# Kernel tuning notes

Measured on AMD Instinct MI355X. Metric: run time of the kernel, lower is better.

The kernel has to match this reference:

```python
import jax, jax.numpy as jnp
import numpy as np
from jax import lax

H_STEP = 1.0 / 3.0  # h = (t1 - t0) / N with t0=0, t1=1, N=3
N_STEPS = 3


def _conv(x, w):
    # x: [B, C, H, W], w: [O, I, kh, kw], 'same' padding, stride 1
    return lax.conv_general_dilated(
        x, w, window_strides=(1, 1), padding='SAME',
        dimension_numbers=('NCHW', 'OIHW', 'NCHW'))


def setup_inputs() -> dict:
    key = jax.random.key(0)
    ks = jax.random.split(key, 5)
    B, C, H, W = 16, 128, 128, 128
    fan_in = C * 9
    return {
        'x': jax.random.normal(ks[0], (B, C, H, W), dtype=jnp.float32),
        'w1': jax.random.normal(ks[1], (C, C, 3, 3), dtype=jnp.float32) * (2.0 / fan_in) ** 0.5,
        'b1': jax.random.normal(ks[2], (C,), dtype=jnp.float32) * 0.01,
        'w2': jax.random.normal(ks[3], (C, C, 3, 3), dtype=jnp.float32) * (2.0 / fan_in) ** 0.5,
        'b2': jax.random.normal(ks[4], (C,), dtype=jnp.float32) * 0.01,
    }


def reference(x, w1, b1, w2, b2):
    # Euler-step residual block: x <- x + h * conv2(relu(conv1(x))) for N steps
    for _ in range(N_STEPS):
        t = jax.nn.relu(_conv(x, w1) + b1[None, :, None, None])
        x = x + H_STEP * (_conv(t, w2) + b2[None, :, None, None])
    return jax.nn.relu(x)
```

## Files before the change

kernel.cpp:

```cpp
#include <hip/hip_runtime.h>
#include <hip/hip_bf16.h>


#define BATCH 16
#define CH    128
#define HH    128
#define WW    128
#define H_STEP (1.0f/3.0f)

typedef short bf16x8 __attribute__((ext_vector_type(8)));
typedef float f32x4  __attribute__((ext_vector_type(4)));

__device__ __forceinline__ float bf2f(unsigned short u) {
    union { unsigned int i; float f; } c; c.i = ((unsigned int)u) << 16; return c.f;
}
__device__ __forceinline__ unsigned short f2bf(float f) {
    union { float f; unsigned int i; } c; c.f = f;
    unsigned int i = c.i;
    return (unsigned short)((i + 0x7FFFu + ((i >> 16) & 1u)) >> 16);
}

__device__ __forceinline__ void gload16(const unsigned short* g, unsigned short* l) {
    __builtin_amdgcn_global_load_lds(
        (const __attribute__((address_space(1))) unsigned int*)g,
        (__attribute__((address_space(3))) unsigned int*)l, 16, 0, 0);
}

__global__ __launch_bounds__(256)
void transpose_x(const float* __restrict__ x, unsigned short* __restrict__ xb)
{
    __shared__ unsigned short s[128 * 132];
    const int tid = threadIdx.x;
    const int bz  = blockIdx.x;
    const int b = bz >> 7, y = bz & 127;

    #pragma unroll
    for (int it = 0; it < 16; ++it) {
        int idx = it * 256 + tid;
        int ci = idx >> 5, xq = idx & 31;
        float4 v = *(const float4*)&x[(((size_t)b * CH + ci) * HH + y) * WW + xq * 4];
        uint2 p;
        p.x = (unsigned int)f2bf(v.x) | ((unsigned int)f2bf(v.y) << 16);
        p.y = (unsigned int)f2bf(v.z) | ((unsigned int)f2bf(v.w) << 16);
        *(uint2*)&s[ci * 132 + xq * 4] = p;
    }
    __syncthreads();
    #pragma unroll
    for (int it = 0; it < 8; ++it) {
        int idx = it * 256 + tid;
        int xx = idx >> 4, cc = idx & 15;
        unsigned short t[8];
        #pragma unroll
        for (int k = 0; k < 8; ++k) t[k] = s[(cc * 8 + k) * 132 + xx];
        uint4 p;
        p.x = (unsigned int)t[0] | ((unsigned int)t[1] << 16);
        p.y = (unsigned int)t[2] | ((unsigned int)t[3] << 16);
        p.z = (unsigned int)t[4] | ((unsigned int)t[5] << 16);
        p.w = (unsigned int)t[6] | ((unsigned int)t[7] << 16);
        *(uint4*)&xb[((size_t)(b * HH + y) * WW + xx) * CH + cc * 8] = p;
    }
}

__global__ __launch_bounds__(256)
void convert_w(const float* __restrict__ w, unsigned short* __restrict__ wb)
{
    int idx = blockIdx.x * 256 + threadIdx.x;
    #pragma unroll
    for (int t = 0; t < 9; ++t)
        wb[t * 16384 + idx] = f2bf(w[(size_t)idx * 9 + t]);
}

template<int MODE>
__global__ __launch_bounds__(256, 2)
void conv_mfma(const unsigned short* __restrict__ in,
               const unsigned short* __restrict__ wb,
               const float* __restrict__ bias,
               const unsigned short* resb,
               unsigned short* outb,
               float* __restrict__ outf)
{
    __shared__ unsigned short s_in[130 * CH];
    __shared__ unsigned short s_w [2][128 * 64];

    const int tid = threadIdx.x;
    const int bz0 = blockIdx.x;
    const int bz  = ((bz0 & 7) << 8) | (bz0 >> 3);
    const int b = bz >> 7, y = bz & 127;

    const int lane = tid & 63;
    const int wid  = tid >> 6;
    const int woc0 = (wid >> 1) * 64;
    const int wpx0 = (wid & 1) * 64;
    const int n16  = lane & 15;
    const int q    = lane >> 4;

    const int wr   = lane >> 3;
    const int wc   = lane & 7;
    const int w_lane_elem = wr * CH + ((wc ^ wr) << 3);
    const int xl   = lane >> 4;
    const int ch16 = lane & 15;

    const int kylo = (y == 0)      ? 1 : 0;
    const int kyhi = (y == HH - 1) ? 1 : 2;
    const int NS   = (kyhi - kylo + 1) * 6;

    f32x4 acc[4][4];
    #pragma unroll
    for (int i = 0; i < 4; ++i)
        #pragma unroll
        for (int j = 0; j < 4; ++j) acc[i][j] = (f32x4)0.0f;

    if (tid < 32) {
        int r  = (tid < 16) ? 0 : 129;
        int cc = tid & 15;
        uint4 z = {0u, 0u, 0u, 0u};
        *(uint4*)&s_in[r * CH + cc * 8] = z;
    }

    auto stage_in = [&](int gy) {
        const size_t inrow = ((size_t)(b * HH + gy) * WW) * CH;
        #pragma unroll
        for (int c = 0; c < 8; ++c) {
            int x   = wid * 32 + c * 4 + xl;
            int swz = (x + 1) & 7;
            const unsigned short* src = in + inrow + (size_t)x * CH + ((ch16 ^ swz) << 3);
            unsigned short* dst = (unsigned short*)s_in + CH + (wid * 8 + c) * 512;
            gload16(src, dst);
        }
    };
    auto stage_w = [&](int tap, int kh, int buf) {
        const unsigned short* wt = wb + tap * 16384 + kh * 64;
        #pragma unroll
        for (int c = 0; c < 4; ++c) {
            int base_r = (wid * 4 + c) * 8;
            const unsigned short* src = wt + base_r * CH + w_lane_elem;
            unsigned short* dst = &s_w[buf][(wid * 4 + c) * 512];
            gload16(src, dst);
        }
    };

    stage_in(y + kylo - 1);
    stage_w(kylo * 3, 0, 0);
    __syncthreads();

    for (int s = 0; s < NS; ++s) {
        const int cur = s & 1;
        const int kyi = s / 6;
        const int r6  = s - kyi * 6;
        const int kx  = r6 >> 1;
        const int kh  = s & 1;

        if (s + 1 < NS) {
            const int s1  = s + 1;
            const int ky1 = s1 / 6;
            const int r61 = s1 - ky1 * 6;
            stage_w((kylo + ky1) * 3 + (r61 >> 1), s1 & 1, cur ^ 1);
        }

        #pragma unroll
        for (int c0 = 0; c0 < 64; c0 += 32) {
            bf16x8 af[4], bfr[4];
            const int cqa = (c0 >> 3) + q;
            #pragma unroll
            for (int i = 0; i < 4; ++i) {
                int row = woc0 + i * 16 + n16;
                af[i] = *(const bf16x8*)&s_w[cur][row * 64 + ((cqa ^ (row & 7)) << 3)];
            }
            const int cqb = kh * 8 + (c0 >> 3) + q;
            #pragma unroll
            for (int j = 0; j < 4; ++j) {
                int rowb = wpx0 + j * 16 + n16 + kx;
                bfr[j] = *(const bf16x8*)&s_in[rowb * CH + ((cqb ^ (rowb & 7)) << 3)];
            }
            #pragma unroll
            for (int i = 0; i < 4; ++i)
                #pragma unroll
                for (int j = 0; j < 4; ++j)
                    acc[i][j] = __builtin_amdgcn_mfma_f32_16x16x32_bf16(
                        af[i], bfr[j], acc[i][j], 0, 0, 0);
        }

        if (r6 == 5 && s + 1 < NS) {
            __syncthreads();
            stage_in(y + (kylo + kyi + 1) - 1);
            __syncthreads();
        } else {
            __syncthreads();
        }
    }

    const int ybase = (b * HH + y) * WW;
    if (MODE == 0 || MODE == 1) {
        #pragma unroll
        for (int j = 0; j < 4; ++j) {
            int x = wpx0 + j * 16 + n16;
            size_t pbase = (size_t)(ybase + x) * CH;
            #pragma unroll
            for (int i = 0; i < 4; ++i) {
                int oc0 = woc0 + i * 16 + q * 4;
                float v0 = acc[i][j][0] + bias[oc0 + 0];
                float v1 = acc[i][j][1] + bias[oc0 + 1];
                float v2 = acc[i][j][2] + bias[oc0 + 2];
                float v3 = acc[i][j][3] + bias[oc0 + 3];
                if (MODE == 0) {
                    v0 = fmaxf(v0, 0.f); v1 = fmaxf(v1, 0.f);
                    v2 = fmaxf(v2, 0.f); v3 = fmaxf(v3, 0.f);
                } else {
                    uint2 rr = *(const uint2*)&resb[pbase + oc0];
                    v0 = bf2f((unsigned short)(rr.x & 0xffff)) + H_STEP * v0;
                    v1 = bf2f((unsigned short)(rr.x >> 16))    + H_STEP * v1;
                    v2 = bf2f((unsigned short)(rr.y & 0xffff)) + H_STEP * v2;
                    v3 = bf2f((unsigned short)(rr.y >> 16))    + H_STEP * v3;
                }
                uint2 po;
                po.x = (unsigned int)f2bf(v0) | ((unsigned int)f2bf(v1) << 16);
                po.y = (unsigned int)f2bf(v2) | ((unsigned int)f2bf(v3) << 16);
                *(uint2*)&outb[pbase + oc0] = po;
            }
        }
    } else {
        #pragma unroll
        for (int i = 0; i < 4; ++i) {
            #pragma unroll
            for (int r = 0; r < 4; ++r) {
                int oc = woc0 + i * 16 + q * 4 + r;
                float bv = bias[oc];
                size_t orow = ((size_t)(b * CH + oc) * HH + y) * WW;
                #pragma unroll
                for (int j = 0; j < 4; ++j) {
                    int x = wpx0 + j * 16 + n16;
                    float v = acc[i][j][r] + bv;
                    v = bf2f(resb[(size_t)(ybase + x) * CH + oc]) + H_STEP * v;
                    outf[orow + x] = fmaxf(v, 0.f);
                }
            }
        }
    }
}

extern "C" void kernel_launch(void* const* d_in, const int* in_sizes, int n_in,
                              void* d_out, int out_size, void* d_ws, size_t ws_size,
                              hipStream_t stream) {
    const float* x0 = (const float*)d_in[0];
    const float* w1 = (const float*)d_in[1];
    const float* b1 = (const float*)d_in[2];
    const float* w2 = (const float*)d_in[3];
    const float* b2 = (const float*)d_in[4];

    const size_t NELEM = (size_t)BATCH * CH * HH * WW;
    unsigned short* XB = (unsigned short*)d_ws;
    unsigned short* T  = XB + NELEM;

    unsigned short* WB1;
    if (ws_size >= NELEM * 4 + 2 * 294912)
        WB1 = T + NELEM;
    else
        WB1 = (unsigned short*)d_in[0];
    unsigned short* WB2 = WB1 + 9 * 16384;

    dim3 block(256);
    dim3 gridRow(BATCH * HH);

    transpose_x<<<gridRow, block, 0, stream>>>(x0, XB);
    convert_w<<<dim3(64), block, 0, stream>>>(w1, WB1);
    convert_w<<<dim3(64), block, 0, stream>>>(w2, WB2);

    conv_mfma<0><<<gridRow, block, 0, stream>>>(XB, WB1, b1, nullptr, T, nullptr);
    conv_mfma<1><<<gridRow, block, 0, stream>>>(T, WB2, b2, XB, XB, nullptr);
    conv_mfma<0><<<gridRow, block, 0, stream>>>(XB, WB1, b1, nullptr, T, nullptr);
    conv_mfma<1><<<gridRow, block, 0, stream>>>(T, WB2, b2, XB, XB, nullptr);
    conv_mfma<0><<<gridRow, block, 0, stream>>>(XB, WB1, b1, nullptr, T, nullptr);
    conv_mfma<2><<<gridRow, block, 0, stream>>>(T, WB2, b2, XB, nullptr, (float*)d_out);
}
```

Before: 800.0 us.

## Halve weight tile K-depth to fit three blocks per CU

Cuts the shared-memory weight stage from 64 to 32 input channels per step, which doubles the number of pipeline steps and barriers. The smaller LDS footprint, together with raising the launch-bounds occupancy hint from 2 to 3, is meant to let three blocks reside per CU for better latency hiding. In exchange there are twice as many __syncthreads and smaller prefetch granules per step, and the higher occupancy target may force register limits on the 64-float accumulator.

```diff
diff --git a/kernel.cpp b/kernel.cpp
--- a/kernel.cpp
+++ b/kernel.cpp
@@ -71,7 +71,7 @@
 }
 
 template<int MODE>
-__global__ __launch_bounds__(256, 2)
+__global__ __launch_bounds__(256, 3)
 void conv_mfma(const unsigned short* __restrict__ in,
                const unsigned short* __restrict__ wb,
                const float* __restrict__ bias,
@@ -80,7 +80,7 @@
                float* __restrict__ outf)
 {
     __shared__ unsigned short s_in[130 * CH];
-    __shared__ unsigned short s_w [2][128 * 64];
+    __shared__ unsigned short s_w [2][128 * 32];
 
     const int tid = threadIdx.x;
     const int bz0 = blockIdx.x;
@@ -94,15 +94,14 @@
     const int n16  = lane & 15;
     const int q    = lane >> 4;
 
-    const int wr   = lane >> 3;
-    const int wc   = lane & 7;
-    const int w_lane_elem = wr * CH + ((wc ^ wr) << 3);
-    const int xl   = lane >> 4;
-    const int ch16 = lane & 15;
+    const int wrow4 = lane >> 2;
+    const int wslot = lane & 3;
+    const int xl    = lane >> 4;
+    const int ch16  = lane & 15;
 
     const int kylo = (y == 0)      ? 1 : 0;
     const int kyhi = (y == HH - 1) ? 1 : 2;
-    const int NS   = (kyhi - kylo + 1) * 6;
+    const int NS   = (kyhi - kylo + 1) * 12;
 
     f32x4 acc[4][4];
     #pragma unroll
@@ -128,13 +127,13 @@
             gload16(src, dst);
         }
     };
-    auto stage_w = [&](int tap, int kh, int buf) {
-        const unsigned short* wt = wb + tap * 16384 + kh * 64;
-        #pragma unroll
-        for (int c = 0; c < 4; ++c) {
-            int base_r = (wid * 4 + c) * 8;
-            const unsigned short* src = wt + base_r * CH + w_lane_elem;
-            unsigned short* dst = &s_w[buf][(wid * 4 + c) * 512];
+    auto stage_w = [&](int tap, int kq, int buf) {
+        const unsigned short* wt = wb + tap * 16384 + kq * 32;
+        #pragma unroll
+        for (int c = 0; c < 2; ++c) {
+            int row = (wid * 2 + c) * 16 + wrow4;
+            const unsigned short* src = wt + row * 128 + ((wslot ^ (row & 3)) << 3);
+            unsigned short* dst = &s_w[buf][(wid * 2 + c) * 512];
             gload16(src, dst);
         }
     };
@@ -143,30 +142,26 @@
     stage_w(kylo * 3, 0, 0);
     __syncthreads();
 
+    int kyi = 0, r12 = 0;
     for (int s = 0; s < NS; ++s) {
         const int cur = s & 1;
-        const int kyi = s / 6;
-        const int r6  = s - kyi * 6;
-        const int kx  = r6 >> 1;
-        const int kh  = s & 1;
-
-        if (s + 1 < NS) {
-            const int s1  = s + 1;
-            const int ky1 = s1 / 6;
-            const int r61 = s1 - ky1 * 6;
-            stage_w((kylo + ky1) * 3 + (r61 >> 1), s1 & 1, cur ^ 1);
-        }
-
-        #pragma unroll
-        for (int c0 = 0; c0 < 64; c0 += 32) {
+        const int kx  = r12 >> 2;
+        const int kq  = r12 & 3;
+
+        int r12n = r12 + 1, kyin = kyi;
+        if (r12n == 12) { r12n = 0; ++kyin; }
+
+        if (s + 1 < NS)
+            stage_w((kylo + kyin) * 3 + (r12n >> 2), r12n & 3, cur ^ 1);
+
+        {
             bf16x8 af[4], bfr[4];
-            const int cqa = (c0 >> 3) + q;
             #pragma unroll
             for (int i = 0; i < 4; ++i) {
                 int row = woc0 + i * 16 + n16;
-                af[i] = *(const bf16x8*)&s_w[cur][row * 64 + ((cqa ^ (row & 7)) << 3)];
-            }
-            const int cqb = kh * 8 + (c0 >> 3) + q;
+                af[i] = *(const bf16x8*)&s_w[cur][row * 32 + ((q ^ (row & 3)) << 3)];
+            }
+            const int cqb = kq * 4 + q;
             #pragma unroll
             for (int j = 0; j < 4; ++j) {
                 int rowb = wpx0 + j * 16 + n16 + kx;
@@ -180,13 +175,14 @@
                         af[i], bfr[j], acc[i][j], 0, 0, 0);
         }
 
-        if (r6 == 5 && s + 1 < NS) {
+        if (r12 == 11 && s + 1 < NS) {
             __syncthreads();
-            stage_in(y + (kylo + kyi + 1) - 1);
+            stage_in(y + kylo + kyi);
             __syncthreads();
         } else {
             __syncthreads();
         }
+        r12 = r12n; kyi = kyin;
     }
 
     const int ybase = (b * HH + y) * WW;
```

Result: no change. 797.6 us (-0.3%).
